# Optimization experiments

Measured on AMD Instinct MI355X. Metric: run time of the kernel, lower is better.

## Reference

```python
import jax, jax.numpy as jnp
import numpy as np
from jax.scipy.special import gammaln

LAG_K = 50  # hard-coded in MLSTMCell


def setup_inputs() -> dict:
    key = jax.random.key(0)
    B, N, H, E = 1024, 50000, 512, 256
    shapes = {
        "enc_w1": (H, N), "enc_b1": (H,), "enc_w2": (E, H), "enc_b2": (E,),
    }
    for g in ("d", "i", "o", "c"):  # u: hidden->input, w: input->input (E==E here)
        shapes[g + "_u_w"] = (E, E); shapes[g + "_u_b"] = (E,)
        shapes[g + "_w_w"] = (E, E); shapes[g + "_w_b"] = (E,)
    shapes.update({"dec_w1": (H, E), "dec_b1": (H,), "dec_w2": (N, H), "dec_b2": (N,)})
    inp = {"x": jax.random.uniform(jax.random.fold_in(key, 0), (B, N + 1), jnp.float32)}
    for i, (nm, sh) in enumerate(shapes.items()):
        scale = 1.0 / np.sqrt(sh[-1]) if len(sh) > 1 else 0.01
        inp[nm] = jax.random.normal(jax.random.fold_in(key, i + 1), sh, jnp.float32) * scale
    return inp


def reference(x, enc_w1, enc_b1, enc_w2, enc_b2,
              d_u_w, d_u_b, d_w_w, d_w_b,
              i_u_w, i_u_b, i_w_w, i_w_b,
              o_u_w, o_u_b, o_w_w, o_w_b,
              c_u_w, c_u_b, c_w_w, c_w_b,
              dec_w1, dec_b1, dec_w2, dec_b2):
    N = enc_w1.shape[1]
    feats = x[:, :N]  # x[:, N] is the node id; all nodes alias ONE shared cell, so ids don't affect math
    # Encoder (DynGEM-style MLP)
    h1 = jax.nn.relu(feats @ enc_w1.T + enc_b1)
    e = jax.nn.relu(h1 @ enc_w2.T + enc_b2)        # [B, E]
    E = e.shape[1]
    kk = jnp.arange(LAG_K, dtype=e.dtype)          # [K]
    lgk1 = gammaln(kk + 1.0)                        # log k!

    # The Python per-batch loop dispatches the SAME shared MLSTM cell sequentially
    # -> sequential recurrence over the batch dim with a lag-K history buffer.
    def step(carry, xt):
        h, hist = carry                             # h [E], hist [K,E] (hist[0] = newest i*c~)
        d = jax.nn.sigmoid(h @ d_u_w.T + d_u_b + xt @ d_w_w.T + d_w_b) * 0.5
        i = jax.nn.sigmoid(h @ i_u_w.T + i_u_b + xt @ i_w_w.T + i_w_b)
        o = jax.nn.sigmoid(h @ o_u_w.T + o_u_b + xt @ o_w_w.T + o_w_b)
        ct = jnp.tanh(h @ c_u_w.T + c_u_b + xt @ c_w_w.T + c_w_b)
        hist = jnp.concatenate([(i * ct)[None, :], hist[:-1]], axis=0)
        # fractional-memory weights: w_k = Gamma(d+k) / (Gamma(k+1) * Gamma(d))
        logw = gammaln(d[None, :] + kk[:, None]) - lgk1[:, None] - gammaln(d)[None, :]
        mem = jnp.sum(jnp.exp(logw) * hist, axis=0)  # zero-padded history == None entries (terms are 0)
        h_new = o * jnp.tanh(mem)
        return (h_new, hist), h_new

    h0 = jnp.zeros((E,), e.dtype)
    hist0 = jnp.zeros((LAG_K, E), e.dtype)
    (_, _), hs = jax.lax.scan(step, (h0, hist0), e)  # hs [B, E]
    # Decoder
    d1 = jax.nn.relu(hs @ dec_w1.T + dec_b1)
    out = jax.nn.sigmoid(d1 @ dec_w2.T + dec_b2)     # [B, N]
    return out
```

## Files before the change

kernel.cpp:

```cpp
#include <hip/hip_runtime.h>

typedef unsigned int u32;
typedef unsigned short u16;
typedef __attribute__((ext_vector_type(4))) u32 u32x4;
typedef __attribute__((ext_vector_type(4))) u16 u16x4;
typedef __attribute__((ext_vector_type(8))) short bf16x8;
typedef __attribute__((ext_vector_type(4))) float f32x4;
typedef __attribute__((ext_vector_type(2))) _Float16 h2f;

#define NSC 8
#define SLICE 32
#define ROWS 128

__device__ __forceinline__ u16 f2bf(float x){
  u32 u = __builtin_bit_cast(u32, x);
  u = (u + 0x7fffu + ((u >> 16) & 1u)) >> 16;
  return (u16)u;
}
__device__ __forceinline__ u16 f2h(float x){
  _Float16 h = (_Float16)x;
  return __builtin_bit_cast(u16, h);
}
__device__ __forceinline__ float h2fl(u16 v){ return (float)__builtin_bit_cast(_Float16, v); }
__device__ __forceinline__ h2f as_h2(u32 v){ return __builtin_bit_cast(h2f, v); }
__device__ __forceinline__ float sigf(float x){ return 1.0f/(1.0f + __expf(-x)); }
__device__ __forceinline__ float tanh_f(float x){ float e = __expf(2.0f*x); return 1.0f - 2.0f/(e + 1.0f); }

__device__ __forceinline__ float dot2acc(u32 a, u32 b, float acc){
#if __has_builtin(__builtin_amdgcn_fdot2)
  return __builtin_amdgcn_fdot2(as_h2(a), as_h2(b), acc, false);
#else
  h2f ha = as_h2(a), hb = as_h2(b);
  return acc + (float)ha[0]*(float)hb[0] + (float)ha[1]*(float)hb[1];
#endif
}
__device__ __forceinline__ float dot4(u32x4 u, u32x4 h, float acc){
  acc = dot2acc(u[0], h[0], acc); acc = dot2acc(u[1], h[1], acc);
  acc = dot2acc(u[2], h[2], acc); acc = dot2acc(u[3], h[3], acc);
  return acc;
}


__global__ void conv_x(const float* __restrict__ x, u16* __restrict__ xb){
  int col4 = (blockIdx.x*256 + threadIdx.x)*4;
  int row  = blockIdx.y;
  const float* src = x + (long)row*50001 + col4;
  u16x4 v;
  if (col4 < 50000) { v[0]=f2bf(src[0]); v[1]=f2bf(src[1]); v[2]=f2bf(src[2]); v[3]=f2bf(src[3]); }
  else { v[0]=0; v[1]=0; v[2]=0; v[3]=0; }
  *(u16x4*)(xb + (long)row*50176 + col4) = v;
}

__global__ void conv_w1(const float* __restrict__ w, u16* __restrict__ wb){
  int col4 = (blockIdx.x*256 + threadIdx.x)*4;
  int row  = blockIdx.y;
  const float* src = w + (long)row*50000 + col4;
  u16x4 v;
  if (col4 < 50000) { v[0]=f2bf(src[0]); v[1]=f2bf(src[1]); v[2]=f2bf(src[2]); v[3]=f2bf(src[3]); }
  else { v[0]=0; v[1]=0; v[2]=0; v[3]=0; }
  *(u16x4*)(wb + (long)row*50176 + col4) = v;
}

__global__ void conv_misc(const float* __restrict__ enc_w2, const float* __restrict__ dec_w1,
                          const float* __restrict__ dw, const float* __restrict__ iw,
                          const float* __restrict__ ow, const float* __restrict__ cw,
                          u16* __restrict__ w2eb, u16* __restrict__ wd1b, u16* __restrict__ wgb){
  int idx = blockIdx.x*256 + threadIdx.x;
  if (idx < 131072) {
    w2eb[idx] = f2bf(enc_w2[idx]);
  } else if (idx < 262144) {
    int i = idx - 131072;
    wd1b[i] = f2bf(dec_w1[i]);
  } else {
    int i = idx - 262144;
    int o = i >> 8, k = i & 255;
    int g = o >> 8, e = o & 255;
    const float* W = (g==0) ? dw : (g==1) ? iw : (g==2) ? ow : cw;
    wgb[i] = f2bf(W[e*256 + k]);
  }
}

__global__ void pack_bias(const float* dub, const float* dwb, const float* iub, const float* iwb,
                          const float* oub, const float* owb, const float* cub, const float* cwb,
                          float* __restrict__ bws){
  int o = blockIdx.x*256 + threadIdx.x;
  int g = o >> 8, e = o & 255;
  float v;
  if      (g==0) v = dub[e] + dwb[e];
  else if (g==1) v = iub[e] + iwb[e];
  else if (g==2) v = oub[e] + owb[e];
  else           v = cub[e] + cwb[e];
  bws[o] = v;
}

__global__ void pack_u(const float* du, const float* iu, const float* ou, const float* cu,
                       u16* __restrict__ upak){
  int b = blockIdx.x;
  int t = threadIdx.x;
  for (int idx = t; idx < ROWS*256; idx += 512) {
    int lr = idx >> 8, k = idx & 255;
    int g = lr >> 5, e = b*SLICE + (lr & 31);
    const float* U = (g==0) ? du : (g==1) ? iu : (g==2) ? ou : cu;
    u16 val = f2h(U[e*256 + k]);
    int dst = lr*256 + ((((k>>3) ^ ((lr>>1)&7)) << 3) | (k & 7));
    upak[b*32768 + dst] = val;
  }
}

template<int EPI>
__global__ __launch_bounds__(256)
void gemm_bt(const u16* __restrict__ A, const u16* __restrict__ B,
             const float* __restrict__ bias, float* __restrict__ Cf, u16* __restrict__ Cb,
             int lda, int ldb, int ldc, int kiters, int nGuard){
  __shared__ u16 As[128*32];
  __shared__ u16 Bs[128*32];
  const int tid = threadIdx.x;
  const int l = tid & 63;
  const int w = tid >> 6;
  const int wr = w >> 1, wc = w & 1;
  const long kchunk = (long)blockIdx.z * kiters * 32;
  const u16* Ab = A + (long)blockIdx.x*128*lda + kchunk;
  const u16* Bb = B + (long)blockIdx.y*128*ldb + kchunk;
  f32x4 acc[4][4];
#pragma unroll
  for (int m=0;m<4;m++)
#pragma unroll
    for (int n=0;n<4;n++) acc[m][n] = (f32x4){0.f,0.f,0.f,0.f};

  const int lr = l & 15, lk = l >> 4;
  for (int it = 0; it < kiters; ++it) {
    {
      int s = tid;
      int row = s >> 2, kg = s & 3;
      u32x4 va = *(const u32x4*)(Ab + (long)row*lda + (long)it*32 + kg*8);
      u32x4 vb = *(const u32x4*)(Bb + (long)row*ldb + (long)it*32 + kg*8);
      int sw = ((kg + row) & 3) * 8;
      *(u32x4*)&As[row*32 + sw] = va;
      *(u32x4*)&Bs[row*32 + sw] = vb;
      s = tid + 256;
      row = s >> 2; kg = s & 3;
      va = *(const u32x4*)(Ab + (long)row*lda + (long)it*32 + kg*8);
      vb = *(const u32x4*)(Bb + (long)row*ldb + (long)it*32 + kg*8);
      sw = ((kg + row) & 3) * 8;
      *(u32x4*)&As[row*32 + sw] = va;
      *(u32x4*)&Bs[row*32 + sw] = vb;
    }
    __syncthreads();
    bf16x8 af[4], bfr[4];
#pragma unroll
    for (int m=0;m<4;m++) {
      int row = wr*64 + m*16 + lr;
      af[m] = *(const bf16x8*)&As[row*32 + (((lk + row)&3)*8)];
    }
#pragma unroll
    for (int n=0;n<4;n++) {
      int row = wc*64 + n*16 + lr;
      bfr[n] = *(const bf16x8*)&Bs[row*32 + (((lk + row)&3)*8)];
    }
#pragma unroll
    for (int m=0;m<4;m++)
#pragma unroll
      for (int n=0;n<4;n++)
        acc[m][n] = __builtin_amdgcn_mfma_f32_16x16x32_bf16(af[m], bfr[n], acc[m][n], 0, 0, 0);
    __syncthreads();
  }
#pragma unroll
  for (int m=0;m<4;m++) {
#pragma unroll
    for (int n=0;n<4;n++) {
#pragma unroll
      for (int v=0;v<4;v++) {
        int r  = wr*64 + m*16 + lk*4 + v;
        int cn = wc*64 + n*16 + lr;
        long gr = (long)blockIdx.x*128 + r;
        long gc = (long)blockIdx.y*128 + cn;
        float val = acc[m][n][v];
        if (EPI == 0) {
          Cf[((long)blockIdx.z*1024 + gr)*ldc + gc] = val;
        } else if (EPI == 1) {
          float y = val + bias[gc];
          y = y > 0.f ? y : 0.f;
          Cb[gr*ldc + gc] = f2bf(y);
        } else if (EPI == 2) {
          Cf[gr*ldc + gc] = val + bias[gc];
        } else if (EPI == 3) {
          if (gc < nGuard) Cf[gr*ldc + gc] = sigf(val + bias[gc]);
        }
      }
    }
  }
}

__global__ void reduce1(const float* __restrict__ P, const float* __restrict__ b1,
                        u16* __restrict__ h1b){
  int idx = blockIdx.x*256 + threadIdx.x;
  float s = b1[idx & 511];
#pragma unroll
  for (int kc = 0; kc < 32; ++kc) s += P[(long)kc*524288 + idx];
  h1b[idx] = f2bf(s > 0.f ? s : 0.f);
}

__global__ __launch_bounds__(512)
void scan_kernel(const u32x4* __restrict__ upak, const float* __restrict__ xw,
                 u16* __restrict__ hsb, const float* __restrict__ dec_w2,
                 u16* __restrict__ w2db, u32* __restrict__ hmail){
  __shared__ __align__(16) u16 U_lds[ROWS*256];
  __shared__ __align__(16) u16 h_lds[256];
  __shared__ float preact[ROWS];
  __shared__ u16   hist[50*34];
  __shared__ float inv_lds[50];
  const int b = blockIdx.x;
  const int t = threadIdx.x;

  if (b >= NSC) {
    const long total = (50048L*512)/4;
    const long stride = (long)(gridDim.x - NSC)*512;
    for (long g2 = (long)(b-NSC)*512 + t; g2 < total; g2 += stride) {
      long base = g2*4;
      long row = base >> 9;
      u16x4 v;
      if (row < 50000) {
        const float* s = dec_w2 + base;
        v[0]=f2bf(s[0]); v[1]=f2bf(s[1]); v[2]=f2bf(s[2]); v[3]=f2bf(s[3]);
      } else { v[0]=0; v[1]=0; v[2]=0; v[3]=0; }
      *(u16x4*)(w2db + base) = v;
    }
    return;
  }

#pragma unroll
  for (int i = 0; i < 8; ++i)
    ((u32x4*)U_lds)[i*512 + t] = upak[b*4096 + i*512 + t];
  for (int i = t; i < 50*34; i += 512) hist[i] = 0;
  if (t < 128) ((u32*)h_lds)[t] = 0;
  if (t < 50) inv_lds[t] = (t == 0) ? 1.0f : (1.0f/(float)t);
  __syncthreads();

  const int kc = t & 7;
  const int rq = t >> 3;
  const int swz = (rq & 7) << 4;
  const int e_loc = t >> 3;
  const int tau = t & 7;
  const int e_glob = b*SLICE + (e_loc & (SLICE-1));

  for (int st = 0; st < 1024; ++st) {
    float xg0=0.f, xg1=0.f, xg2=0.f, xg3=0.f;
    if (t < 256) {
      xg0 = xw[st*1024 +       e_glob];
      xg1 = xw[st*1024 + 256 + e_glob];
      xg2 = xw[st*1024 + 512 + e_glob];
      xg3 = xw[st*1024 + 768 + e_glob];
    }
    if (st > 0) {
      if (t < 256) {
        const u32* wp = hmail + ((st&1)<<8) + t;
        u32 v;
        do {
          v = __hip_atomic_load(wp, __ATOMIC_RELAXED, __HIP_MEMORY_SCOPE_AGENT);
        } while ((v >> 16) != (u32)st);
        h_lds[t] = (u16)v;
      }
      __syncthreads();
    }
    float a0 = 0.f, a1 = 0.f;
#pragma unroll
    for (int p = 0; p < 4; ++p) {
      u32x4 hb = *(const u32x4*)((const char*)h_lds + kc*64 + p*16);
      u32x4 u0 = *(const u32x4*)((const char*)U_lds + (2*rq  )*512 + ((kc*64 + p*16) ^ swz));
      u32x4 u1 = *(const u32x4*)((const char*)U_lds + (2*rq+1)*512 + ((kc*64 + p*16) ^ swz));
      a0 = dot4(u0, hb, a0);
      a1 = dot4(u1, hb, a1);
    }
    a0 += __shfl_xor(a0,1); a0 += __shfl_xor(a0,2); a0 += __shfl_xor(a0,4);
    a1 += __shfl_xor(a1,1); a1 += __shfl_xor(a1,2); a1 += __shfl_xor(a1,4);
    if (kc == 0) { preact[2*rq] = a0; preact[2*rq+1] = a1; }
    __syncthreads();

    if (t < 256) {
      float pd = preact[0*SLICE + e_loc] + xg0;
      float pi = preact[1*SLICE + e_loc] + xg1;
      float po = preact[2*SLICE + e_loc] + xg2;
      float pc = preact[3*SLICE + e_loc] + xg3;
      float d  = 0.5f * sigf(pd);
      float gi = sigf(pi);
      float go = sigf(po);
      float ct = tanh_f(pc);
      float cur = gi * ct;
      float c = 1.f;
      if (tau < 7) {
#pragma unroll
        for (int m = 0; m < 7; ++m) {
          int j = 7*tau + m;
          c *= (d + (float)j) * inv_lds[j+1];
        }
      }
      float v = c;
      float s1 = __shfl_up(v,1,8); if (tau >= 1) v *= s1;
      float s2 = __shfl_up(v,2,8); if (tau >= 2) v *= s2;
      float s4 = __shfl_up(v,4,8); if (tau >= 4) v *= s4;
      float S = __shfl_up(v,1,8); if (tau == 0) S = 1.f;
      int base = st % 50;
      float r = S, memp = 0.f;
      if (tau < 7) {
#pragma unroll
        for (int m = 0; m < 7; ++m) {
          int k = 7*tau + 1 + m;
          r *= (d + (float)(k-1)) * inv_lds[k];
          int sl = base - k; if (sl < 0) sl += 50;
          memp += r * h2fl(hist[sl*34 + e_loc]);
        }
      }
      memp += __shfl_xor(memp,1,8); memp += __shfl_xor(memp,2,8); memp += __shfl_xor(memp,4,8);
      float mem = memp + cur;
      float hnew = go * tanh_f(mem);
      if (tau == 0) {
        __hip_atomic_store(hmail + ((((st+1)&1))<<8) + e_glob,
                           (((u32)(st+1)) << 16) | (u32)f2h(hnew),
                           __ATOMIC_RELAXED, __HIP_MEMORY_SCOPE_AGENT);
        hist[base*34 + e_loc] = f2h(cur);
        hsb[st*256 + e_glob] = f2bf(hnew);
      }
    }
  }
}

extern "C" void kernel_launch(void* const* d_in, const int* in_sizes, int n_in,
                              void* d_out, int out_size, void* d_ws, size_t ws_size,
                              hipStream_t stream){
  const float* x      = (const float*)d_in[0];
  const float* enc_w1 = (const float*)d_in[1];
  const float* enc_b1 = (const float*)d_in[2];
  const float* enc_w2 = (const float*)d_in[3];
  const float* enc_b2 = (const float*)d_in[4];
  const float* d_u_w  = (const float*)d_in[5];  const float* d_u_b = (const float*)d_in[6];
  const float* d_w_w  = (const float*)d_in[7];  const float* d_w_b = (const float*)d_in[8];
  const float* i_u_w  = (const float*)d_in[9];  const float* i_u_b = (const float*)d_in[10];
  const float* i_w_w  = (const float*)d_in[11]; const float* i_w_b = (const float*)d_in[12];
  const float* o_u_w  = (const float*)d_in[13]; const float* o_u_b = (const float*)d_in[14];
  const float* o_w_w  = (const float*)d_in[15]; const float* o_w_b = (const float*)d_in[16];
  const float* c_u_w  = (const float*)d_in[17]; const float* c_u_b = (const float*)d_in[18];
  const float* c_w_w  = (const float*)d_in[19]; const float* c_w_b = (const float*)d_in[20];
  const float* dec_w1 = (const float*)d_in[21]; const float* dec_b1 = (const float*)d_in[22];
  const float* dec_w2 = (const float*)d_in[23]; const float* dec_b2 = (const float*)d_in[24];

  char* ws = (char*)d_ws;
  u16*   xb     = (u16*)(ws + 0L);
  u16*   w1b    = (u16*)(ws + 102760448L);
  u16*   w2db   = (u16*)(ws + 154140672L);
  u16*   h1b    = (u16*)(ws + 205389824L);
  u16*   e_b    = (u16*)(ws + 206438400L);
  u16*   wgb    = (u16*)(ws + 206962688L);
  u16*   w2eb   = (u16*)(ws + 207486976L);
  u16*   wd1b   = (u16*)(ws + 207749120L);
  u16*   d1b    = (u16*)(ws + 208011264L);
  u16*   hsb    = (u16*)(ws + 209059840L);
  float* xw     = (float*)(ws + 209584128L);
  float* bws    = (float*)(ws + 213778432L);
  u16*   upak   = (u16*)(ws + 213782528L);
  float* out    = (float*)d_out;
  float* P      = (float*)d_out;
  u32*   hmail  = (u32*)((char*)d_out + 200000000L);

  hipMemsetAsync(hmail, 0, 2048, stream);

  conv_x   <<<dim3(49,1024), 256, 0, stream>>>(x, xb);
  conv_w1  <<<dim3(49,512),  256, 0, stream>>>(enc_w1, w1b);
  conv_misc<<<2048, 256, 0, stream>>>(enc_w2, dec_w1, d_w_w, i_w_w, o_w_w, c_w_w, w2eb, wd1b, wgb);
  pack_bias<<<4, 256, 0, stream>>>(d_u_b, d_w_b, i_u_b, i_w_b, o_u_b, o_w_b, c_u_b, c_w_b, bws);
  pack_u   <<<NSC, 512, 0, stream>>>(d_u_w, i_u_w, o_u_w, c_u_w, upak);

  gemm_bt<0><<<dim3(8,4,32), 256, 0, stream>>>(xb, w1b, nullptr, P, nullptr, 50176, 50176, 512, 49, 0);
  reduce1<<<2048, 256, 0, stream>>>(P, enc_b1, h1b);
  gemm_bt<1><<<dim3(8,2,1), 256, 0, stream>>>(h1b, w2eb, enc_b2, nullptr, e_b, 512, 512, 256, 16, 0);
  gemm_bt<2><<<dim3(8,8,1), 256, 0, stream>>>(e_b, wgb, bws, xw, nullptr, 256, 256, 1024, 8, 0);
  scan_kernel<<<197, 512, 0, stream>>>((const u32x4*)upak, xw, hsb, dec_w2, w2db, hmail);
  gemm_bt<1><<<dim3(8,4,1), 256, 0, stream>>>(hsb, wd1b, dec_b1, nullptr, d1b, 256, 256, 512, 8, 0);
  gemm_bt<3><<<dim3(8,391,1), 256, 0, stream>>>(d1b, w2db, dec_b2, out, nullptr, 512, 512, 50000, 16, 50000);
}
```

Before: 2.869 ms.

## Co-locate scan workgroups on one XCC and use L2-scoped mailbox polling

Result: slower. 9.389 ms (+227.3%).

```diff
diff --git a/kernel.cpp b/kernel.cpp
--- a/kernel.cpp
+++ b/kernel.cpp
@@ -209,13 +209,37 @@
   __shared__ float preact[ROWS];
   __shared__ u16   hist[50*34];
   __shared__ float inv_lds[50];
-  const int b = blockIdx.x;
+  __shared__ int   s_role, s_rank;
   const int t = threadIdx.x;
-
-  if (b >= NSC) {
+  u32* const ectr = hmail + 1024;
+
+  if (t == 0) {
+    u32 xcc;
+    asm volatile("s_getreg_b32 %0, hwreg(HW_REG_XCC_ID)" : "=s"(xcc));
+    u32 g = __hip_atomic_fetch_add(ectr+0, 1u, __ATOMIC_RELAXED, __HIP_MEMORY_SCOPE_AGENT);
+    if (g == 0)
+      __hip_atomic_store(ectr+1, xcc+1u, __ATOMIC_RELEASE, __HIP_MEMORY_SCOPE_AGENT);
+    u32 chosen;
+    do { chosen = __hip_atomic_load(ectr+1, __ATOMIC_ACQUIRE, __HIP_MEMORY_SCOPE_AGENT); }
+    while (chosen == 0);
+    int role = 1, rank;
+    if (xcc == chosen-1u) {
+      u32 s = __hip_atomic_fetch_add(ectr+2, 1u, __ATOMIC_RELAXED, __HIP_MEMORY_SCOPE_AGENT);
+      if (s < NSC) { role = 0; rank = (int)s; }
+      else rank = (int)__hip_atomic_fetch_add(ectr+3, 1u, __ATOMIC_RELAXED, __HIP_MEMORY_SCOPE_AGENT);
+    } else {
+      rank = (int)__hip_atomic_fetch_add(ectr+3, 1u, __ATOMIC_RELAXED, __HIP_MEMORY_SCOPE_AGENT);
+    }
+    s_role = role; s_rank = rank;
+  }
+  __syncthreads();
+  const int role = s_role;
+  const int b    = s_rank;
+
+  if (role != 0) {
     const long total = (50048L*512)/4;
     const long stride = (long)(gridDim.x - NSC)*512;
-    for (long g2 = (long)(b-NSC)*512 + t; g2 < total; g2 += stride) {
+    for (long g2 = (long)b*512 + t; g2 < total; g2 += stride) {
       long base = g2*4;
       long row = base >> 9;
       u16x4 v;
@@ -253,11 +277,18 @@
     }
     if (st > 0) {
       if (t < 256) {
-        const u32* wp = hmail + ((st&1)<<8) + t;
-        u32 v;
-        do {
-          v = __hip_atomic_load(wp, __ATOMIC_RELAXED, __HIP_MEMORY_SCOPE_AGENT);
-        } while ((v >> 16) != (u32)st);
+        const u32* fp = hmail + ((st&1)<<8) + t;
+        const u32* sp = fp + 512;
+        u32 v; int spins = 0;
+        for (;;) {
+          asm volatile("global_load_dword %0, %1, off sc0\n\ts_waitcnt vmcnt(0)"
+                       : "=v"(v) : "v"(fp));
+          if ((v >> 16) == (u32)st) break;
+          if (__builtin_expect(++spins > 64, 0)) {
+            v = __hip_atomic_load(sp, __ATOMIC_RELAXED, __HIP_MEMORY_SCOPE_AGENT);
+            if ((v >> 16) == (u32)st) break;
+          }
+        }
         h_lds[t] = (u16)v;
       }
       __syncthreads();
@@ -314,9 +345,10 @@
       float mem = memp + cur;
       float hnew = go * tanh_f(mem);
       if (tau == 0) {
-        __hip_atomic_store(hmail + ((((st+1)&1))<<8) + e_glob,
-                           (((u32)(st+1)) << 16) | (u32)f2h(hnew),
-                           __ATOMIC_RELAXED, __HIP_MEMORY_SCOPE_AGENT);
+        u32 pv = (((u32)(st+1)) << 16) | (u32)f2h(hnew);
+        u32* fp = hmail + ((((st+1)&1))<<8) + e_glob;
+        asm volatile("global_store_dword %0, %1, off" :: "v"(fp), "v"(pv) : "memory");
+        __hip_atomic_store(fp + 512, pv, __ATOMIC_RELAXED, __HIP_MEMORY_SCOPE_AGENT);
         hist[base*34 + e_loc] = f2h(cur);
         hsb[st*256 + e_glob] = f2bf(hnew);
       }
@@ -361,7 +393,7 @@
   float* P      = (float*)d_out;
   u32*   hmail  = (u32*)((char*)d_out + 200000000L);
 
-  hipMemsetAsync(hmail, 0, 2048, stream);
+  hipMemsetAsync(hmail, 0, 8192, stream);
 
   conv_x   <<<dim3(49,1024), 256, 0, stream>>>(x, xb);
   conv_w1  <<<dim3(49,512),  256, 0, stream>>>(enc_w1, w1b);
```

## Keep recurrent U weights in registers and prefetch next-step gate inputs

Applied to the files above, without the earlier changes.

Measured after the change: 2.810 ms, median of 2. 1.02x faster.

```diff
diff --git a/kernel.cpp b/kernel.cpp
--- a/kernel.cpp
+++ b/kernel.cpp
@@ -94,16 +94,20 @@
 }
 
 __global__ void pack_u(const float* du, const float* iu, const float* ou, const float* cu,
-                       u16* __restrict__ upak){
+                       u32* __restrict__ upak){
   int b = blockIdx.x;
   int t = threadIdx.x;
-  for (int idx = t; idx < ROWS*256; idx += 512) {
-    int lr = idx >> 8, k = idx & 255;
+  int rq = t >> 3, kc = t & 7;
+  for (int q = 0; q < 8; ++q) {
+    int lr = 2*rq + (q >> 2);
     int g = lr >> 5, e = b*SLICE + (lr & 31);
     const float* U = (g==0) ? du : (g==1) ? iu : (g==2) ? ou : cu;
-    u16 val = f2h(U[e*256 + k]);
-    int dst = lr*256 + ((((k>>3) ^ ((lr>>1)&7)) << 3) | (k & 7));
-    upak[b*32768 + dst] = val;
+    const float* row = U + e*256 + kc*32 + (q & 3)*8;
+    for (int p = 0; p < 4; ++p) {
+      u32 lo = f2h(row[p*2]);
+      u32 hi = f2h(row[p*2+1]);
+      upak[((long)(b*512 + t)*8 + q)*4 + p] = lo | (hi << 16);
+    }
   }
 }
 
@@ -200,12 +204,11 @@
   h1b[idx] = f2bf(s > 0.f ? s : 0.f);
 }
 
-__global__ __launch_bounds__(512)
-void scan_kernel(const u32x4* __restrict__ upak, const float* __restrict__ xw,
+__global__ __launch_bounds__(512) __attribute__((amdgpu_waves_per_eu(2,2)))
+void scan_kernel(const u32* __restrict__ upak, const float* __restrict__ xw,
                  u16* __restrict__ hsb, const float* __restrict__ dec_w2,
                  u16* __restrict__ w2db, u32* __restrict__ hmail){
-  __shared__ __align__(16) u16 U_lds[ROWS*256];
-  __shared__ __align__(16) u16 h_lds[256];
+  __shared__ __align__(16) u16 h_lds[320];
   __shared__ float preact[ROWS];
   __shared__ u16   hist[50*34];
   __shared__ float inv_lds[50];
@@ -228,29 +231,33 @@
     return;
   }
 
-#pragma unroll
-  for (int i = 0; i < 8; ++i)
-    ((u32x4*)U_lds)[i*512 + t] = upak[b*4096 + i*512 + t];
-  for (int i = t; i < 50*34; i += 512) hist[i] = 0;
-  if (t < 128) ((u32*)h_lds)[t] = 0;
-  if (t < 50) inv_lds[t] = (t == 0) ? 1.0f : (1.0f/(float)t);
-  __syncthreads();
-
   const int kc = t & 7;
   const int rq = t >> 3;
-  const int swz = (rq & 7) << 4;
   const int e_loc = t >> 3;
   const int tau = t & 7;
   const int e_glob = b*SLICE + (e_loc & (SLICE-1));
 
+  const long ubase = (long)(b*512 + t)*32;
+  u32x4 Uq0 = *(const u32x4*)(upak + ubase + 0);
+  u32x4 Uq1 = *(const u32x4*)(upak + ubase + 4);
+  u32x4 Uq2 = *(const u32x4*)(upak + ubase + 8);
+  u32x4 Uq3 = *(const u32x4*)(upak + ubase + 12);
+  u32x4 Uq4 = *(const u32x4*)(upak + ubase + 16);
+  u32x4 Uq5 = *(const u32x4*)(upak + ubase + 20);
+  u32x4 Uq6 = *(const u32x4*)(upak + ubase + 24);
+  u32x4 Uq7 = *(const u32x4*)(upak + ubase + 28);
+
+  for (int i = t; i < 50*34; i += 512) hist[i] = 0;
+  if (t < 320) h_lds[t] = 0;
+  if (t < 50) inv_lds[t] = (t == 0) ? 1.0f : (1.0f/(float)t);
+  __syncthreads();
+
+  float xg0=0.f, xg1=0.f, xg2=0.f, xg3=0.f;
+  if (t < 256) {
+    xg0 = xw[e_glob]; xg1 = xw[256 + e_glob]; xg2 = xw[512 + e_glob]; xg3 = xw[768 + e_glob];
+  }
+
   for (int st = 0; st < 1024; ++st) {
-    float xg0=0.f, xg1=0.f, xg2=0.f, xg3=0.f;
-    if (t < 256) {
-      xg0 = xw[st*1024 +       e_glob];
-      xg1 = xw[st*1024 + 256 + e_glob];
-      xg2 = xw[st*1024 + 512 + e_glob];
-      xg3 = xw[st*1024 + 768 + e_glob];
-    }
     if (st > 0) {
       if (t < 256) {
         const u32* wp = hmail + ((st&1)<<8) + t;
@@ -258,22 +265,29 @@
         do {
           v = __hip_atomic_load(wp, __ATOMIC_RELAXED, __HIP_MEMORY_SCOPE_AGENT);
         } while ((v >> 16) != (u32)st);
-        h_lds[t] = (u16)v;
+        h_lds[(t>>5)*40 + (t&31)] = (u16)v;
       }
       __syncthreads();
     }
-    float a0 = 0.f, a1 = 0.f;
-#pragma unroll
-    for (int p = 0; p < 4; ++p) {
-      u32x4 hb = *(const u32x4*)((const char*)h_lds + kc*64 + p*16);
-      u32x4 u0 = *(const u32x4*)((const char*)U_lds + (2*rq  )*512 + ((kc*64 + p*16) ^ swz));
-      u32x4 u1 = *(const u32x4*)((const char*)U_lds + (2*rq+1)*512 + ((kc*64 + p*16) ^ swz));
-      a0 = dot4(u0, hb, a0);
-      a1 = dot4(u1, hb, a1);
-    }
-    a0 += __shfl_xor(a0,1); a0 += __shfl_xor(a0,2); a0 += __shfl_xor(a0,4);
-    a1 += __shfl_xor(a1,1); a1 += __shfl_xor(a1,2); a1 += __shfl_xor(a1,4);
-    if (kc == 0) { preact[2*rq] = a0; preact[2*rq+1] = a1; }
+    float xn0=0.f, xn1=0.f, xn2=0.f, xn3=0.f;
+    if (st < 1023 && t < 256) {
+      const float* xp = xw + (st+1)*1024;
+      xn0 = xp[e_glob]; xn1 = xp[256 + e_glob]; xn2 = xp[512 + e_glob]; xn3 = xp[768 + e_glob];
+    }
+    {
+      u32x4 hb0 = *(const u32x4*)((const char*)h_lds + kc*80 +  0);
+      u32x4 hb1 = *(const u32x4*)((const char*)h_lds + kc*80 + 16);
+      u32x4 hb2 = *(const u32x4*)((const char*)h_lds + kc*80 + 32);
+      u32x4 hb3 = *(const u32x4*)((const char*)h_lds + kc*80 + 48);
+      float a0 = 0.f, a1 = 0.f;
+      a0 = dot4(Uq0, hb0, a0); a0 = dot4(Uq1, hb1, a0);
+      a0 = dot4(Uq2, hb2, a0); a0 = dot4(Uq3, hb3, a0);
+      a1 = dot4(Uq4, hb0, a1); a1 = dot4(Uq5, hb1, a1);
+      a1 = dot4(Uq6, hb2, a1); a1 = dot4(Uq7, hb3, a1);
+      a0 += __shfl_xor(a0,1); a0 += __shfl_xor(a0,2); a0 += __shfl_xor(a0,4);
+      a1 += __shfl_xor(a1,1); a1 += __shfl_xor(a1,2); a1 += __shfl_xor(a1,4);
+      if (kc == 0) { preact[2*rq] = a0; preact[2*rq+1] = a1; }
+    }
     __syncthreads();
 
     if (t < 256) {
@@ -321,6 +335,7 @@
         hsb[st*256 + e_glob] = f2bf(hnew);
       }
     }
+    xg0 = xn0; xg1 = xn1; xg2 = xn2; xg3 = xn3;
   }
 }
 
@@ -356,7 +371,7 @@
   u16*   hsb    = (u16*)(ws + 209059840L);
   float* xw     = (float*)(ws + 209584128L);
   float* bws    = (float*)(ws + 213778432L);
-  u16*   upak   = (u16*)(ws + 213782528L);
+  u32*   upak   = (u32*)(ws + 213782528L);
   float* out    = (float*)d_out;
   float* P      = (float*)d_out;
   u32*   hmail  = (u32*)((char*)d_out + 200000000L);
@@ -373,7 +388,7 @@
   reduce1<<<2048, 256, 0, stream>>>(P, enc_b1, h1b);
   gemm_bt<1><<<dim3(8,2,1), 256, 0, stream>>>(h1b, w2eb, enc_b2, nullptr, e_b, 512, 512, 256, 16, 0);
   gemm_bt<2><<<dim3(8,8,1), 256, 0, stream>>>(e_b, wgb, bws, xw, nullptr, 256, 256, 1024, 8, 0);
-  scan_kernel<<<197, 512, 0, stream>>>((const u32x4*)upak, xw, hsb, dec_w2, w2db, hmail);
+  scan_kernel<<<197, 512, 0, stream>>>(upak, xw, hsb, dec_w2, w2db, hmail);
   gemm_bt<1><<<dim3(8,4,1), 256, 0, stream>>>(hsb, wd1b, dec_b1, nullptr, d1b, 256, 256, 512, 8, 0);
   gemm_bt<3><<<dim3(8,391,1), 256, 0, stream>>>(d1b, w2db, dec_b2, out, nullptr, 512, 512, 50000, 16, 50000);
 }
```
